# Optimization experiments

Measured on AMD Instinct MI355X. Metric: run time of the kernel, lower is better.

## Reference

```python
import jax, jax.numpy as jnp
import numpy as np

NEG = 0.01  # leaky_relu negative slope

def leaky(x):
    return jax.nn.leaky_relu(x, NEG)

def mlp3(x, W0, b0, W1, b1, W2, b2):
    h = leaky(x @ W0 + b0)
    h = leaky(h @ W1 + b1)
    return h @ W2 + b2

B_, T_, N_FINE, F_IN = 2, 4, 64800, 78
N_COARSE, E_LAT, H, D_OUT = 842, 5894, 256, 256

def setup_inputs() -> dict:
    key = jax.random.key(0)
    ks = jax.random.split(key, 24)
    def lin(k, i, o):
        return jax.random.normal(k, (i, o), jnp.float32) * 0.02, jnp.zeros((o,), jnp.float32)
    x = jax.random.normal(ks[0], (B_, T_, N_FINE, F_IN), jnp.float32)
    # one edge per fine node: src = node index, dst = its coarse h3 cell
    edge_index = jnp.stack([jnp.arange(N_FINE, dtype=jnp.int32),
                            jax.random.randint(ks[1], (N_FINE,), 0, N_COARSE, dtype=jnp.int32)])
    edge_attr = 2.0 * jax.random.uniform(ks[2], (N_FINE, 2), jnp.float32) - 1.0  # [sin d, cos d]
    latent_edge_index = jax.random.randint(ks[3], (2, E_LAT), 0, N_COARSE, dtype=jnp.int32)
    latent_edge_attr = 2.0 * jax.random.uniform(ks[4], (E_LAT, 2), jnp.float32) - 1.0
    h3_nodes = jax.random.normal(ks[5], (N_COARSE, F_IN), jnp.float32) * 0.02
    eW0, eb0 = lin(ks[6], 2 * F_IN + 2, H); eW1, eb1 = lin(ks[7], H, H); eW2, eb2 = lin(ks[8], H, D_OUT)
    nW0, nb0 = lin(ks[9], F_IN + D_OUT, H); nW1, nb1 = lin(ks[10], H, H); nW2, nb2 = lin(ks[11], H, D_OUT)
    rW0, rb0 = lin(ks[12], 2, H); rW1, rb1 = lin(ks[13], H, H); rW2, rb2 = lin(ks[14], H, D_OUT)
    rWs, rbs = lin(ks[15], 2, D_OUT)
    return dict(x=x, edge_index=edge_index, edge_attr=edge_attr,
                latent_edge_index=latent_edge_index, latent_edge_attr=latent_edge_attr,
                h3_nodes=h3_nodes,
                eW0=eW0, eb0=eb0, eW1=eW1, eb1=eb1, eW2=eW2, eb2=eb2,
                nW0=nW0, nb0=nb0, nW1=nW1, nb1=nb1, nW2=nW2, nb2=nb2,
                rW0=rW0, rb0=rb0, rW1=rW1, rb1=rb1, rW2=rW2, rb2=rb2,
                rWs=rWs, rbs=rbs)

def reference(x, edge_index, edge_attr, latent_edge_index, latent_edge_attr, h3_nodes,
              eW0, eb0, eW1, eb1, eW2, eb2,
              nW0, nb0, nW1, nb1, nW2, nb2,
              rW0, rb0, rW1, rb1, rW2, rb2, rWs, rbs):
    b, t, n, f = x.shape
    B = b * t
    xf = x.reshape(B, n, f)                      # (b t) n f
    src, dst = edge_index[0], edge_index[1]      # [E]
    nc = h3_nodes.shape[0]
    E = src.shape[0]
    # --- edge MLP: gather src fine feats, dst latent feats, edge attrs ---
    e_in = jnp.concatenate([
        xf[:, src],                                          # [B,E,f]
        jnp.broadcast_to(h3_nodes[dst][None], (B, E, f)),    # [B,E,f]
        jnp.broadcast_to(edge_attr[None], (B, E, 2)),        # [B,E,2]
    ], axis=-1)
    msgs = mlp3(e_in, eW0, eb0, eW1, eb1, eW2, eb2)          # [B,E,D]
    # --- scatter-sum to coarse nodes ---
    agg = jax.vmap(lambda m: jax.ops.segment_sum(m, dst, num_segments=nc))(msgs)  # [B,nc,D]
    # --- node MLP on concat(latent nodes, aggregated messages) ---
    n_in = jnp.concatenate([jnp.broadcast_to(h3_nodes[None], (B, nc, f)), agg], axis=-1)
    nodes = mlp3(n_in, nW0, nb0, nW1, nb1, nW2, nb2)          # [B,nc,D]
    nodes = nodes.reshape(b, t, nc, -1)
    # --- residual MLP over latent edge attrs (eval: dropout off, parametrized skip) ---
    h = leaky(latent_edge_attr @ rW0 + rb0)
    h = leaky(h @ rW1 + rb1)
    attrs = h @ rW2 + rb2 + (latent_edge_attr @ rWs + rbs)
    return (nodes, latent_edge_index, attrs)
```

## Files before the change

kernel.cpp:

```cpp
#include <hip/hip_runtime.h>

#define E_EDGES 64800
#define NC      842
#define NB      8
#define FIN     78
#define E_LAT   5894
#define NROWS_NODE (NB*NC)
#define EPB      16
#define NTILES_E 4050
#define TAIL_B   192

#define OUT_IDX_OFF   1724416
#define OUT_IDX_N     11788
#define OUT_ATTR_OFF  1736204

#define AGG_OFF    0
#define CNT_OFF    6897664
#define CUR_OFF    6901032
#define SSRC_OFF   6904400
#define SDST_OFF   7163600
#define SATTR_OFF  7293200
#define WPACK_OFF  7811600

#define WOFF_E0 0
#define WOFF_E1 40960
#define WOFF_E2 106496
#define WOFF_N0 172032
#define WOFF_N1 262144
#define WOFF_N2 327680
#define WOFF_R0 393216
#define WOFF_R1 401408
#define WOFF_R2 466944

#define SH   262
#define SA_N 362

typedef __bf16 bf16x8 __attribute__((ext_vector_type(8)));
typedef float  f32x4  __attribute__((ext_vector_type(4)));

__device__ __forceinline__ unsigned short f2bf(float f) {
    unsigned u = __builtin_bit_cast(unsigned, f);
    return (unsigned short)((u + 0x7fffu + ((u >> 16) & 1u)) >> 16);
}
__device__ __forceinline__ unsigned packRTZ(float lo, float hi) {
    return __builtin_amdgcn_perm(__builtin_bit_cast(unsigned, hi),
                                 __builtin_bit_cast(unsigned, lo), 0x07060302u);
}

template<int MF>
__device__ __forceinline__ void zero_acc(f32x4 (&acc)[MF][4]) {
#pragma unroll
    for (int mf = 0; mf < MF; ++mf)
#pragma unroll
        for (int nf = 0; nf < 4; ++nf)
            acc[mf][nf] = (f32x4){0.f, 0.f, 0.f, 0.f};
}

template<int MF, int NKS>
__device__ __forceinline__ void run_layer(const unsigned short* lA, int strideA,
                                          const unsigned short* Wp, int nfg0,
                                          int m15, int q, f32x4 (&acc)[MF][4]) {
    const unsigned short* wp0 = Wp + (size_t)nfg0 * 512 + (threadIdx.x & 63) * 8;
    bf16x8 bcur[4], bnxt[4];
#pragma unroll
    for (int nf = 0; nf < 4; ++nf) bcur[nf] = *(const bf16x8*)(wp0 + nf * 512);
#pragma unroll
    for (int kk = 0; kk < NKS; ++kk) {
        if (kk + 1 < NKS) {
#pragma unroll
            for (int nf = 0; nf < 4; ++nf)
                bnxt[nf] = *(const bf16x8*)(wp0 + (size_t)(kk + 1) * 16 * 512 + nf * 512);
        }
        bf16x8 a[MF];
#pragma unroll
        for (int mf = 0; mf < MF; ++mf)
            a[mf] = *(const bf16x8*)(lA + (mf * 16 + m15) * strideA + kk * 32 + q * 8);
#pragma unroll
        for (int nf = 0; nf < 4; ++nf)
#pragma unroll
            for (int mf = 0; mf < MF; ++mf)
                acc[mf][nf] = __builtin_amdgcn_mfma_f32_16x16x32_bf16(a[mf], bcur[nf], acc[mf][nf], 0, 0, 0);
#pragma unroll
        for (int nf = 0; nf < 4; ++nf) bcur[nf] = bnxt[nf];
    }
}

template<int MF>
__device__ __forceinline__ void epi_act(unsigned short* Sb, int stride, const f32x4 (&acc)[MF][4],
                                        const float* bias, int w, int m15, int q) {
#pragma unroll
    for (int nf = 0; nf < 4; ++nf) {
        int col = w * 64 + nf * 16 + m15;
        float bv = bias[col];
#pragma unroll
        for (int mf = 0; mf < MF; ++mf)
#pragma unroll
            for (int r4 = 0; r4 < 4; ++r4) {
                int row = mf * 16 + q * 4 + r4;
                float y = acc[mf][nf][r4] + bv;
                y = fmaxf(y, 0.01f * y);
                Sb[row * stride + col] = (unsigned short)(__builtin_bit_cast(unsigned, y) >> 16);
            }
    }
}

__global__ void pack_weights(const float* s0, const float* s1, const float* s2,
                             const float* s3, const float* s4, const float* s5,
                             const float* s6, const float* s7, const float* s8,
                             unsigned short* wp) {
    const int ksA[9]  = {5, 8, 8, 11, 8, 8, 1, 8, 8};
    const int kaA[9]  = {158, 256, 256, 334, 256, 256, 2, 256, 256};
    const int offA[9] = {WOFF_E0, WOFF_E1, WOFF_E2, WOFF_N0, WOFF_N1, WOFF_N2,
                         WOFF_R0, WOFF_R1, WOFF_R2};
    const float* srcs[9] = {s0, s1, s2, s3, s4, s5, s6, s7, s8};
    int rem = blockIdx.x;
    int l = 0;
    while (rem >= ksA[l] * 16) { rem -= ksA[l] * 16; ++l; }
    int kk = rem >> 4, nf = rem & 15;
    int lane = threadIdx.x >> 3, j = threadIdx.x & 7;
    int k = kk * 32 + (lane >> 4) * 8 + j;
    int n = nf * 16 + (lane & 15);
    float v = (k < kaA[l]) ? srcs[l][k * 256 + n] : 0.f;
    wp[(size_t)offA[l] + (size_t)(kk * 16 + nf) * 512 + lane * 8 + j] = f2bf(v);
}

__global__ void hist_kernel(const int* __restrict__ dstA, int* __restrict__ cnt) {
    int e = blockIdx.x * 256 + threadIdx.x;
    if (e < E_EDGES) atomicAdd(&cnt[dstA[e]], 1);
}
__global__ void scan_kernel(const int* __restrict__ cnt, int* __restrict__ cursor) {
    __shared__ int s[1024];
    int t = threadIdx.x;
    s[t] = (t < NC) ? cnt[t] : 0;
    __syncthreads();
    for (int d = 1; d < 1024; d <<= 1) {
        int v = (t >= d) ? s[t - d] : 0;
        __syncthreads();
        s[t] += v;
        __syncthreads();
    }
    if (t < NC) cursor[t] = (t == 0) ? 0 : s[t - 1];
}
__global__ void scatter_kernel(const int* __restrict__ srcA, const int* __restrict__ dstA,
                               const float* __restrict__ eattr, int* __restrict__ cursor,
                               int* __restrict__ ssrc, short* __restrict__ sdst,
                               float2* __restrict__ sattr) {
    int e = blockIdx.x * 256 + threadIdx.x;
    if (e < E_EDGES) {
        int d = dstA[e];
        int p = atomicAdd(&cursor[d], 1);
        ssrc[p] = srcA[e];
        sdst[p] = (short)d;
        sattr[p] = ((const float2*)eattr)[e];
    }
}

__global__ __launch_bounds__(256, 2) void edge_mlp_kernel(
    const float* __restrict__ x, const float* __restrict__ h3,
    const float* __restrict__ eb0, const float* __restrict__ eb1, const float* __restrict__ eb2,
    const unsigned short* __restrict__ wpack, const int* __restrict__ ssrc,
    const short* __restrict__ sdst, const float2* __restrict__ sattr,
    float* __restrict__ agg,
    const float* __restrict__ la, const float* __restrict__ rb0,
    const float* __restrict__ rb1, const float* __restrict__ rb2,
    const float* __restrict__ rWs, const float* __restrict__ rbs,
    const int* __restrict__ lei, float* __restrict__ out) {
    __shared__ __align__(16) unsigned short S[128 * SH];
    __shared__ short dstl[EPB];
    __shared__ int   srcl[EPB];
    __shared__ unsigned char starts[EPB + 4];
    __shared__ int nseg;

    const int tid = threadIdx.x, lane = tid & 63, w = tid >> 6;
    const int m15 = lane & 15, q = lane >> 4;

    if (blockIdx.x >= NTILES_E) {
        const int blk = blockIdx.x - NTILES_E;
        if (blk >= 185) {
            for (int i = (blk - 185) * 256 + tid; i < OUT_IDX_N; i += 7 * 256)
                out[OUT_IDX_OFF + i] = (float)lei[i];
            return;
        }
        const int base = blk * 32;
        {
            const int rr = tid >> 3, j = tid & 7;
            unsigned short* Sr = S + rr * SH;
            unsigned v0 = 0;
            if (j == 0 && base + rr < E_LAT) {
                float2 f = *(const float2*)(la + (size_t)(base + rr) * 2);
                v0 = packRTZ(f.x, f.y);
            }
            *(unsigned*)(Sr + 2 * j) = v0;
            *(unsigned*)(Sr + 2 * (j + 8)) = 0;
        }
        __syncthreads();

        f32x4 acc[2][4];
        zero_acc<2>(acc);
        run_layer<2, 1>(S, SH, wpack + WOFF_R0, w * 4, m15, q, acc);
        __syncthreads();
        epi_act<2>(S, SH, acc, rb0, w, m15, q);
        __syncthreads();

        zero_acc<2>(acc);
        run_layer<2, 8>(S, SH, wpack + WOFF_R1, w * 4, m15, q, acc);
        __syncthreads();
        epi_act<2>(S, SH, acc, rb1, w, m15, q);
        __syncthreads();

        zero_acc<2>(acc);
        run_layer<2, 8>(S, SH, wpack + WOFF_R2, w * 4, m15, q, acc);

        float* outA = out + OUT_ATTR_OFF;
#pragma unroll
        for (int nf = 0; nf < 4; ++nf) {
            int col = w * 64 + nf * 16 + m15;
            float bv = rb2[col] + rbs[col];
            float ws0 = rWs[col], ws1 = rWs[256 + col];
#pragma unroll
            for (int mf = 0; mf < 2; ++mf)
#pragma unroll
                for (int r4 = 0; r4 < 4; ++r4) {
                    int row = mf * 16 + q * 4 + r4;
                    int e = base + row;
                    if (e < E_LAT) {
                        float v = acc[mf][nf][r4] + bv + la[e * 2] * ws0 + la[e * 2 + 1] * ws1;
                        outA[(size_t)e * 256 + col] = v;
                    }
                }
        }
        return;
    }

    const int base = blockIdx.x * EPB;

    if (tid < EPB) {
        dstl[tid] = sdst[base + tid];
        srcl[tid] = ssrc[base + tid];
    }
    __syncthreads();

    if (tid == 0) {
        int ns = 0; short prev = -2;
        for (int r = 0; r < EPB; ++r) {
            short d = dstl[r];
            if (d != prev) { starts[ns++] = (unsigned char)r; prev = d; }
        }
        starts[ns] = EPB;
        nseg = ns;
    }

    {
        const int rr = tid >> 3, j = tid & 7;
#pragma unroll
        for (int pass = 0; pass < 4; ++pass) {
            const int row = pass * 32 + rr;
            const int b = row >> 4, e = row & 15;
            const float* xr = x + ((size_t)b * E_EDGES + srcl[e]) * FIN;
            const float* hr = h3 + (int)dstl[e] * FIN;
            unsigned short* Sr = S + row * SH;
#pragma unroll
            for (int t = 0; t < 5; ++t) {
                int p = j + 8 * t;
                if (p < 39) {
                    float2 f = *(const float2*)(xr + 2 * p);
                    float2 g = *(const float2*)(hr + 2 * p);
                    *(unsigned*)(Sr + 2 * p) = packRTZ(f.x, f.y);
                    *(unsigned*)(Sr + 78 + 2 * p) = packRTZ(g.x, g.y);
                } else if (p == 39) {
                    float2 a2 = sattr[base + e];
                    *(unsigned*)(Sr + 156) = packRTZ(a2.x, a2.y);
                    *(unsigned*)(Sr + 158) = 0;
                }
            }
        }
    }
    float bnf[4];
#pragma unroll
    for (int nf = 0; nf < 4; ++nf) bnf[nf] = eb2[w * 64 + nf * 16 + m15];
    __syncthreads();

    f32x4 acc[8][4];
    zero_acc<8>(acc);
    run_layer<8, 5>(S, SH, wpack + WOFF_E0, w * 4, m15, q, acc);
    __syncthreads();
    epi_act<8>(S, SH, acc, eb0, w, m15, q);
    __syncthreads();

    zero_acc<8>(acc);
    run_layer<8, 8>(S, SH, wpack + WOFF_E1, w * 4, m15, q, acc);
    __syncthreads();
    epi_act<8>(S, SH, acc, eb1, w, m15, q);
    __syncthreads();

    zero_acc<8>(acc);
    run_layer<8, 8>(S, SH, wpack + WOFF_E2, w * 4, m15, q, acc);

    const int ns = nseg;
#pragma unroll
    for (int nf = 0; nf < 4; ++nf) {
        for (int s = 0; s < ns; ++s) {
            const int lo = starts[s], hi = starts[s + 1];
            const int dc = dstl[lo];
#pragma unroll
            for (int mf = 0; mf < 8; ++mf) {
                float t = 0.f;
#pragma unroll
                for (int r4 = 0; r4 < 4; ++r4) {
                    int e = q * 4 + r4;
                    t += (e >= lo && e < hi) ? acc[mf][nf][r4] : 0.f;
                }
                t += __shfl_xor(t, 16, 64);
                t += __shfl_xor(t, 32, 64);
                if (q == nf) {
                    atomicAdd(&agg[((size_t)mf * NC + dc) * 256 + w * 64 + nf * 16 + m15],
                              t + bnf[nf] * (float)(hi - lo));
                }
            }
        }
    }
}

__global__ __launch_bounds__(256, 4) void node_mlp_kernel(
    const float* __restrict__ h3, const float* __restrict__ agg,
    const float* __restrict__ nb0, const float* __restrict__ nb1, const float* __restrict__ nb2,
    const unsigned short* __restrict__ wpack, float* __restrict__ out) {
    __shared__ __align__(16) unsigned short S[16 * SA_N];

    const int base = blockIdx.x * 16;
    const int tid = threadIdx.x, lane = tid & 63, w = tid >> 6;
    const int m15 = lane & 15, q = lane >> 4;

    {
        const int rr = tid >> 4, l16 = tid & 15;
        const int jj = base + rr;
        const int vl = jj < NROWS_NODE;
        const int c = vl ? jj % NC : 0;
        const float* hr = h3 + c * FIN;
        const float* ar = agg + (size_t)jj * 256;
        unsigned short* Sr = S + rr * SA_N;
#pragma unroll
        for (int t = 0; t < 12; ++t) {
            int p = l16 + 16 * t;
            if (p < 39) {
                float2 f = *(const float2*)(hr + 2 * p);
                *(unsigned*)(Sr + 2 * p) = packRTZ(f.x, f.y);
            } else if (p < 167) {
                unsigned v = 0;
                if (vl) { float2 f = *(const float2*)(ar + 2 * p - 78); v = packRTZ(f.x, f.y); }
                *(unsigned*)(Sr + 2 * p) = v;
            } else if (p < 176) {
                *(unsigned*)(Sr + 2 * p) = 0;
            }
        }
    }
    __syncthreads();

    f32x4 acc[1][4];
    zero_acc<1>(acc);
    run_layer<1, 11>(S, SA_N, wpack + WOFF_N0, w * 4, m15, q, acc);
    __syncthreads();
    epi_act<1>(S, SA_N, acc, nb0, w, m15, q);
    __syncthreads();

    zero_acc<1>(acc);
    run_layer<1, 8>(S, SA_N, wpack + WOFF_N1, w * 4, m15, q, acc);
    __syncthreads();
    epi_act<1>(S, SA_N, acc, nb1, w, m15, q);
    __syncthreads();

    zero_acc<1>(acc);
    run_layer<1, 8>(S, SA_N, wpack + WOFF_N2, w * 4, m15, q, acc);

#pragma unroll
    for (int nf = 0; nf < 4; ++nf) {
        int col = w * 64 + nf * 16 + m15;
        float bv = nb2[col];
#pragma unroll
        for (int r4 = 0; r4 < 4; ++r4) {
            int jj = base + q * 4 + r4;
            if (jj < NROWS_NODE) out[(size_t)jj * 256 + col] = acc[0][nf][r4] + bv;
        }
    }
}

extern "C" void kernel_launch(void* const* d_in, const int* in_sizes, int n_in,
                              void* d_out, int out_size, void* d_ws, size_t ws_size,
                              hipStream_t stream) {
    const float* x      = (const float*)d_in[0];
    const int*   eidx   = (const int*)d_in[1];
    const float* eattr  = (const float*)d_in[2];
    const int*   lei    = (const int*)d_in[3];
    const float* la     = (const float*)d_in[4];
    const float* h3     = (const float*)d_in[5];
    const float* eW0 = (const float*)d_in[6],  *eb0 = (const float*)d_in[7];
    const float* eW1 = (const float*)d_in[8],  *eb1 = (const float*)d_in[9];
    const float* eW2 = (const float*)d_in[10], *eb2 = (const float*)d_in[11];
    const float* nW0 = (const float*)d_in[12], *nb0 = (const float*)d_in[13];
    const float* nW1 = (const float*)d_in[14], *nb1 = (const float*)d_in[15];
    const float* nW2 = (const float*)d_in[16], *nb2 = (const float*)d_in[17];
    const float* rW0 = (const float*)d_in[18], *rb0 = (const float*)d_in[19];
    const float* rW1 = (const float*)d_in[20], *rb1 = (const float*)d_in[21];
    const float* rW2 = (const float*)d_in[22], *rb2 = (const float*)d_in[23];
    const float* rWs = (const float*)d_in[24], *rbs = (const float*)d_in[25];

    char* ws = (char*)d_ws;
    float* agg    = (float*)(ws + AGG_OFF);
    int* cnt      = (int*)(ws + CNT_OFF);
    int* cur      = (int*)(ws + CUR_OFF);
    int* ssrc     = (int*)(ws + SSRC_OFF);
    short* sdst   = (short*)(ws + SDST_OFF);
    float2* sattr = (float2*)(ws + SATTR_OFF);
    unsigned short* wpack = (unsigned short*)(ws + WPACK_OFF);

    float* out = (float*)d_out;

    hipMemsetAsync(d_ws, 0, CUR_OFF, stream);

    pack_weights<<<1040, 512, 0, stream>>>(eW0, eW1, eW2, nW0, nW1, nW2, rW0, rW1, rW2, wpack);
    hist_kernel<<<254, 256, 0, stream>>>(eidx + E_EDGES, cnt);
    scan_kernel<<<1, 1024, 0, stream>>>(cnt, cur);
    scatter_kernel<<<254, 256, 0, stream>>>(eidx, eidx + E_EDGES, eattr, cur,
                                            ssrc, sdst, sattr);
    edge_mlp_kernel<<<NTILES_E + TAIL_B, 256, 0, stream>>>(
        x, h3, eb0, eb1, eb2, wpack, ssrc, sdst, sattr, agg,
        la, rb0, rb1, rb2, rWs, rbs, lei, out);
    node_mlp_kernel<<<421, 256, 0, stream>>>(h3, agg, nb0, nb1, nb2, wpack, out);
}
```

Measured before the change: 733.0 us.

## Make edge MLP persistent with register-resident weights and merge node/tail kernels

The edge MLP becomes a persistent kernel of 256 blocks with 512 threads. Each wave loads its 32-column slice of all three edge-layer weights into registers once, then loops over 8-edge tiles (64 rows across the 8 batches). This removes the repeated weight streaming from global memory on every tile. The latent-edge residual MLP and the index copy move out of the edge kernel into a combined node/tail kernel. The trade-offs are heavy register pressure under a 512-thread, 2-block launch bound, which may cause spills, and roughly twice as many atomic segment flushes from the smaller tiles.

```diff
diff --git a/kernel.cpp b/kernel.cpp
--- a/kernel.cpp
+++ b/kernel.cpp
@@ -6,8 +6,10 @@
 #define FIN     78
 #define E_LAT   5894
 #define NROWS_NODE (NB*NC)
-#define EPB      16
-#define NTILES_E 4050
+#define EPB      8
+#define NT_EDGE  8100
+#define EDGE_GRID 256
+#define NODE_B   421
 #define TAIL_B   192
 
 #define OUT_IDX_OFF   1724416
@@ -47,13 +49,31 @@
                                  __builtin_bit_cast(unsigned, lo), 0x07060302u);
 }
 
-template<int MF>
-__device__ __forceinline__ void zero_acc(f32x4 (&acc)[MF][4]) {
+template<int MF, int NF>
+__device__ __forceinline__ void zero_acc(f32x4 (&acc)[MF][NF]) {
 #pragma unroll
     for (int mf = 0; mf < MF; ++mf)
 #pragma unroll
-        for (int nf = 0; nf < 4; ++nf)
+        for (int nf = 0; nf < NF; ++nf)
             acc[mf][nf] = (f32x4){0.f, 0.f, 0.f, 0.f};
+}
+
+template<int MF, int NKS>
+__device__ __forceinline__ void run_layer_reg(const unsigned short* lA, int strideA,
+                                              const bf16x8 (&wr)[NKS][2],
+                                              int m15, int q, f32x4 (&acc)[MF][2]) {
+#pragma unroll
+    for (int kk = 0; kk < NKS; ++kk) {
+        bf16x8 a[MF];
+#pragma unroll
+        for (int mf = 0; mf < MF; ++mf)
+            a[mf] = *(const bf16x8*)(lA + (mf * 16 + m15) * strideA + kk * 32 + q * 8);
+#pragma unroll
+        for (int nf = 0; nf < 2; ++nf)
+#pragma unroll
+            for (int mf = 0; mf < MF; ++mf)
+                acc[mf][nf] = __builtin_amdgcn_mfma_f32_16x16x32_bf16(a[mf], wr[kk][nf], acc[mf][nf], 0, 0, 0);
+    }
 }
 
 template<int MF, int NKS>
@@ -85,12 +105,12 @@
     }
 }
 
-template<int MF>
-__device__ __forceinline__ void epi_act(unsigned short* Sb, int stride, const f32x4 (&acc)[MF][4],
-                                        const float* bias, int w, int m15, int q) {
-#pragma unroll
-    for (int nf = 0; nf < 4; ++nf) {
-        int col = w * 64 + nf * 16 + m15;
+template<int MF, int NF>
+__device__ __forceinline__ void epi_act(unsigned short* Sb, int stride, const f32x4 (&acc)[MF][NF],
+                                        const float* bias, int colbase, int m15, int q) {
+#pragma unroll
+    for (int nf = 0; nf < NF; ++nf) {
+        int col = colbase + nf * 16 + m15;
         float bv = bias[col];
 #pragma unroll
         for (int mf = 0; mf < MF; ++mf)
@@ -155,27 +175,138 @@
     }
 }
 
-__global__ __launch_bounds__(256, 2) void edge_mlp_kernel(
+__global__ __launch_bounds__(512, 2) void edge_mlp_kernel(
     const float* __restrict__ x, const float* __restrict__ h3,
     const float* __restrict__ eb0, const float* __restrict__ eb1, const float* __restrict__ eb2,
     const unsigned short* __restrict__ wpack, const int* __restrict__ ssrc,
     const short* __restrict__ sdst, const float2* __restrict__ sattr,
-    float* __restrict__ agg,
+    float* __restrict__ agg) {
+    __shared__ __align__(16) unsigned short S[64 * SH];
+    __shared__ short dstl[EPB];
+    __shared__ unsigned char starts[EPB + 4];
+    __shared__ int nseg;
+
+    const int tid = threadIdx.x, lane = tid & 63, w = tid >> 6;
+    const int m15 = lane & 15, q = lane >> 4;
+
+    const unsigned short* wb = wpack + (size_t)(w * 2) * 512 + lane * 8;
+    bf16x8 wE0[5][2], wE1[8][2], wE2[8][2];
+#pragma unroll
+    for (int kk = 0; kk < 5; ++kk)
+#pragma unroll
+        for (int nf = 0; nf < 2; ++nf)
+            wE0[kk][nf] = *(const bf16x8*)(wb + WOFF_E0 + (kk * 16 + nf) * 512);
+#pragma unroll
+    for (int kk = 0; kk < 8; ++kk)
+#pragma unroll
+        for (int nf = 0; nf < 2; ++nf) {
+            wE1[kk][nf] = *(const bf16x8*)(wb + WOFF_E1 + (kk * 16 + nf) * 512);
+            wE2[kk][nf] = *(const bf16x8*)(wb + WOFF_E2 + (kk * 16 + nf) * 512);
+        }
+    float bnf[2];
+#pragma unroll
+    for (int nf = 0; nf < 2; ++nf) bnf[nf] = eb2[w * 32 + nf * 16 + m15];
+
+    const int rr = tid >> 3, j = tid & 7;
+    const int sb = rr >> 3, se = rr & 7;
+    const int ebase = (q & 1) * 4;
+    const int bh = q >> 1;
+
+    for (int t = blockIdx.x; t < NT_EDGE; t += gridDim.x) {
+        const int base = t * EPB;
+        __syncthreads();
+
+        if (tid < EPB) dstl[tid] = sdst[base + tid];
+        if (tid == 0) {
+            int ns = 0; short prev = -2;
+            for (int r = 0; r < EPB; ++r) {
+                short d = sdst[base + r];
+                if (d != prev) { starts[ns++] = (unsigned char)r; prev = d; }
+            }
+            starts[ns] = EPB;
+            nseg = ns;
+        }
+
+        {
+            const int eg = base + se;
+            const float* xr = x + ((size_t)sb * E_EDGES + ssrc[eg]) * FIN;
+            const float* hr = h3 + (int)sdst[eg] * FIN;
+            unsigned short* Sr = S + rr * SH;
+#pragma unroll
+            for (int tt = 0; tt < 5; ++tt) {
+                int p = j + 8 * tt;
+                if (p < 39) {
+                    float2 f = *(const float2*)(xr + 2 * p);
+                    float2 g = *(const float2*)(hr + 2 * p);
+                    *(unsigned*)(Sr + 2 * p) = packRTZ(f.x, f.y);
+                    *(unsigned*)(Sr + 78 + 2 * p) = packRTZ(g.x, g.y);
+                } else if (p == 39) {
+                    float2 a2 = sattr[eg];
+                    *(unsigned*)(Sr + 156) = packRTZ(a2.x, a2.y);
+                    *(unsigned*)(Sr + 158) = 0;
+                }
+            }
+        }
+        __syncthreads();
+
+        f32x4 acc[4][2];
+        zero_acc(acc);
+        run_layer_reg<4, 5>(S, SH, wE0, m15, q, acc);
+        __syncthreads();
+        epi_act(S, SH, acc, eb0, w * 32, m15, q);
+        __syncthreads();
+
+        zero_acc(acc);
+        run_layer_reg<4, 8>(S, SH, wE1, m15, q, acc);
+        __syncthreads();
+        epi_act(S, SH, acc, eb1, w * 32, m15, q);
+        __syncthreads();
+
+        zero_acc(acc);
+        run_layer_reg<4, 8>(S, SH, wE2, m15, q, acc);
+
+        const int ns = nseg;
+#pragma unroll
+        for (int nf = 0; nf < 2; ++nf) {
+            const float bv = bnf[nf];
+            for (int s = 0; s < ns; ++s) {
+                const int lo = starts[s], hi = starts[s + 1];
+                const int dc = dstl[lo];
+#pragma unroll
+                for (int mf = 0; mf < 4; ++mf) {
+                    float tv = 0.f;
+#pragma unroll
+                    for (int r4 = 0; r4 < 4; ++r4) {
+                        int e = ebase + r4;
+                        tv += (e >= lo && e < hi) ? acc[mf][nf][r4] : 0.f;
+                    }
+                    tv += __shfl_xor(tv, 16, 64);
+                    if ((q & 1) == 0) {
+                        atomicAdd(&agg[((size_t)(2 * mf + bh) * NC + dc) * 256
+                                       + w * 32 + nf * 16 + m15],
+                                  tv + bv * (float)(hi - lo));
+                    }
+                }
+            }
+        }
+    }
+}
+
+__global__ __launch_bounds__(256, 4) void node_tail_kernel(
+    const float* __restrict__ h3, const float* __restrict__ agg,
+    const float* __restrict__ nb0, const float* __restrict__ nb1, const float* __restrict__ nb2,
+    const unsigned short* __restrict__ wpack, float* __restrict__ out,
     const float* __restrict__ la, const float* __restrict__ rb0,
     const float* __restrict__ rb1, const float* __restrict__ rb2,
     const float* __restrict__ rWs, const float* __restrict__ rbs,
-    const int* __restrict__ lei, float* __restrict__ out) {
-    __shared__ __align__(16) unsigned short S[128 * SH];
-    __shared__ short dstl[EPB];
-    __shared__ int   srcl[EPB];
-    __shared__ unsigned char starts[EPB + 4];
-    __shared__ int nseg;
+    const int* __restrict__ lei) {
+    __shared__ __align__(16) unsigned short S[32 * SH];
 
     const int tid = threadIdx.x, lane = tid & 63, w = tid >> 6;
     const int m15 = lane & 15, q = lane >> 4;
 
-    if (blockIdx.x >= NTILES_E) {
-        const int blk = blockIdx.x - NTILES_E;
+    if (blockIdx.x >= NODE_B) {
+        const int blk = blockIdx.x - NODE_B;
         if (blk >= 185) {
             for (int i = (blk - 185) * 256 + tid; i < OUT_IDX_N; i += 7 * 256)
                 out[OUT_IDX_OFF + i] = (float)lei[i];
@@ -183,32 +314,32 @@
         }
         const int base = blk * 32;
         {
-            const int rr = tid >> 3, j = tid & 7;
+            const int rr = tid >> 3, jj = tid & 7;
             unsigned short* Sr = S + rr * SH;
             unsigned v0 = 0;
-            if (j == 0 && base + rr < E_LAT) {
+            if (jj == 0 && base + rr < E_LAT) {
                 float2 f = *(const float2*)(la + (size_t)(base + rr) * 2);
                 v0 = packRTZ(f.x, f.y);
             }
-            *(unsigned*)(Sr + 2 * j) = v0;
-            *(unsigned*)(Sr + 2 * (j + 8)) = 0;
+            *(unsigned*)(Sr + 2 * jj) = v0;
+            *(unsigned*)(Sr + 2 * (jj + 8)) = 0;
         }
         __syncthreads();
 
         f32x4 acc[2][4];
-        zero_acc<2>(acc);
+        zero_acc(acc);
         run_layer<2, 1>(S, SH, wpack + WOFF_R0, w * 4, m15, q, acc);
         __syncthreads();
-        epi_act<2>(S, SH, acc, rb0, w, m15, q);
-        __syncthreads();
-
-        zero_acc<2>(acc);
+        epi_act(S, SH, acc, rb0, w * 64, m15, q);
+        __syncthreads();
+
+        zero_acc(acc);
         run_layer<2, 8>(S, SH, wpack + WOFF_R1, w * 4, m15, q, acc);
         __syncthreads();
-        epi_act<2>(S, SH, acc, rb1, w, m15, q);
-        __syncthreads();
-
-        zero_acc<2>(acc);
+        epi_act(S, SH, acc, rb1, w * 64, m15, q);
+        __syncthreads();
+
+        zero_acc(acc);
         run_layer<2, 8>(S, SH, wpack + WOFF_R2, w * 4, m15, q, acc);
 
         float* outA = out + OUT_ATTR_OFF;
@@ -232,104 +363,7 @@
         return;
     }
 
-    const int base = blockIdx.x * EPB;
-
-    if (tid < EPB) {
-        dstl[tid] = sdst[base + tid];
-        srcl[tid] = ssrc[base + tid];
-    }
-    __syncthreads();
-
-    if (tid == 0) {
-        int ns = 0; short prev = -2;
-        for (int r = 0; r < EPB; ++r) {
-            short d = dstl[r];
-            if (d != prev) { starts[ns++] = (unsigned char)r; prev = d; }
-        }
-        starts[ns] = EPB;
-        nseg = ns;
-    }
-
-    {
-        const int rr = tid >> 3, j = tid & 7;
-#pragma unroll
-        for (int pass = 0; pass < 4; ++pass) {
-            const int row = pass * 32 + rr;
-            const int b = row >> 4, e = row & 15;
-            const float* xr = x + ((size_t)b * E_EDGES + srcl[e]) * FIN;
-            const float* hr = h3 + (int)dstl[e] * FIN;
-            unsigned short* Sr = S + row * SH;
-#pragma unroll
-            for (int t = 0; t < 5; ++t) {
-                int p = j + 8 * t;
-                if (p < 39) {
-                    float2 f = *(const float2*)(xr + 2 * p);
-                    float2 g = *(const float2*)(hr + 2 * p);
-                    *(unsigned*)(Sr + 2 * p) = packRTZ(f.x, f.y);
-                    *(unsigned*)(Sr + 78 + 2 * p) = packRTZ(g.x, g.y);
-                } else if (p == 39) {
-                    float2 a2 = sattr[base + e];
-                    *(unsigned*)(Sr + 156) = packRTZ(a2.x, a2.y);
-                    *(unsigned*)(Sr + 158) = 0;
-                }
-            }
-        }
-    }
-    float bnf[4];
-#pragma unroll
-    for (int nf = 0; nf < 4; ++nf) bnf[nf] = eb2[w * 64 + nf * 16 + m15];
-    __syncthreads();
-
-    f32x4 acc[8][4];
-    zero_acc<8>(acc);
-    run_layer<8, 5>(S, SH, wpack + WOFF_E0, w * 4, m15, q, acc);
-    __syncthreads();
-    epi_act<8>(S, SH, acc, eb0, w, m15, q);
-    __syncthreads();
-
-    zero_acc<8>(acc);
-    run_layer<8, 8>(S, SH, wpack + WOFF_E1, w * 4, m15, q, acc);
-    __syncthreads();
-    epi_act<8>(S, SH, acc, eb1, w, m15, q);
-    __syncthreads();
-
-    zero_acc<8>(acc);
-    run_layer<8, 8>(S, SH, wpack + WOFF_E2, w * 4, m15, q, acc);
-
-    const int ns = nseg;
-#pragma unroll
-    for (int nf = 0; nf < 4; ++nf) {
-        for (int s = 0; s < ns; ++s) {
-            const int lo = starts[s], hi = starts[s + 1];
-            const int dc = dstl[lo];
-#pragma unroll
-            for (int mf = 0; mf < 8; ++mf) {
-                float t = 0.f;
-#pragma unroll
-                for (int r4 = 0; r4 < 4; ++r4) {
-                    int e = q * 4 + r4;
-                    t += (e >= lo && e < hi) ? acc[mf][nf][r4] : 0.f;
-                }
-                t += __shfl_xor(t, 16, 64);
-                t += __shfl_xor(t, 32, 64);
-                if (q == nf) {
-                    atomicAdd(&agg[((size_t)mf * NC + dc) * 256 + w * 64 + nf * 16 + m15],
-                              t + bnf[nf] * (float)(hi - lo));
-                }
-            }
-        }
-    }
-}
-
-__global__ __launch_bounds__(256, 4) void node_mlp_kernel(
-    const float* __restrict__ h3, const float* __restrict__ agg,
-    const float* __restrict__ nb0, const float* __restrict__ nb1, const float* __restrict__ nb2,
-    const unsigned short* __restrict__ wpack, float* __restrict__ out) {
-    __shared__ __align__(16) unsigned short S[16 * SA_N];
-
     const int base = blockIdx.x * 16;
-    const int tid = threadIdx.x, lane = tid & 63, w = tid >> 6;
-    const int m15 = lane & 15, q = lane >> 4;
 
     {
         const int rr = tid >> 4, l16 = tid & 15;
@@ -340,8 +374,8 @@
         const float* ar = agg + (size_t)jj * 256;
         unsigned short* Sr = S + rr * SA_N;
 #pragma unroll
-        for (int t = 0; t < 12; ++t) {
-            int p = l16 + 16 * t;
+        for (int tt = 0; tt < 12; ++tt) {
+            int p = l16 + 16 * tt;
             if (p < 39) {
                 float2 f = *(const float2*)(hr + 2 * p);
                 *(unsigned*)(Sr + 2 * p) = packRTZ(f.x, f.y);
@@ -357,19 +391,19 @@
     __syncthreads();
 
     f32x4 acc[1][4];
-    zero_acc<1>(acc);
+    zero_acc(acc);
     run_layer<1, 11>(S, SA_N, wpack + WOFF_N0, w * 4, m15, q, acc);
     __syncthreads();
-    epi_act<1>(S, SA_N, acc, nb0, w, m15, q);
-    __syncthreads();
-
-    zero_acc<1>(acc);
+    epi_act(S, SA_N, acc, nb0, w * 64, m15, q);
+    __syncthreads();
+
+    zero_acc(acc);
     run_layer<1, 8>(S, SA_N, wpack + WOFF_N1, w * 4, m15, q, acc);
     __syncthreads();
-    epi_act<1>(S, SA_N, acc, nb1, w, m15, q);
-    __syncthreads();
-
-    zero_acc<1>(acc);
+    epi_act(S, SA_N, acc, nb1, w * 64, m15, q);
+    __syncthreads();
+
+    zero_acc(acc);
     run_layer<1, 8>(S, SA_N, wpack + WOFF_N2, w * 4, m15, q, acc);
 
 #pragma unroll
@@ -422,8 +456,9 @@
     scan_kernel<<<1, 1024, 0, stream>>>(cnt, cur);
     scatter_kernel<<<254, 256, 0, stream>>>(eidx, eidx + E_EDGES, eattr, cur,
                                             ssrc, sdst, sattr);
-    edge_mlp_kernel<<<NTILES_E + TAIL_B, 256, 0, stream>>>(
-        x, h3, eb0, eb1, eb2, wpack, ssrc, sdst, sattr, agg,
-        la, rb0, rb1, rb2, rWs, rbs, lei, out);
-    node_mlp_kernel<<<421, 256, 0, stream>>>(h3, agg, nb0, nb1, nb2, wpack, out);
-}
+    edge_mlp_kernel<<<EDGE_GRID, 512, 0, stream>>>(x, h3, eb0, eb1, eb2,
+                                                   wpack, ssrc, sdst, sattr, agg);
+    node_tail_kernel<<<NODE_B + TAIL_B, 256, 0, stream>>>(
+        h3, agg, nb0, nb1, nb2, wpack, out,
+        la, rb0, rb1, rb2, rWs, rbs, lei);
+}
```

Measured after the change: 1.062 ms. +44.8%, slower.
